# Performance work log

Measured on AMD Instinct MI355X. Metric: run time of the kernel, lower is better.

The kernel has to match this reference:

```python
import jax, jax.numpy as jnp
import numpy as np

IN_FEATURES = 4096
OUT_FEATURES = 4096
RANK = 16
ALPHA = 32.0
SCALING = ALPHA / RANK


def setup_inputs() -> dict:
    key = jax.random.key(0)
    k_x, k_a, k_b = jax.random.split(key, 3)
    x = jax.random.normal(k_x, (4, 2048, IN_FEATURES), dtype=jnp.float32)
    # kaiming-uniform(a=sqrt(5)) for A: bound = sqrt(6/((1+5)*fan_in)) = 1/sqrt(fan_in)
    bound = 1.0 / np.sqrt(IN_FEATURES)
    lora_A = jax.random.uniform(k_a, (RANK, IN_FEATURES), dtype=jnp.float32,
                                minval=-bound, maxval=bound)
    # B is zero-init in the module; use small random values so gradients are non-trivial
    lora_B = jax.random.normal(k_b, (OUT_FEATURES, RANK), dtype=jnp.float32) * 0.01
    return {"x": x, "lora_A": lora_A, "lora_B": lora_B}


def reference(x, lora_A, lora_B):
    # dropout=0 -> identity. F.linear(x, B@A) == x @ A^T @ B^T; keep low-rank order.
    h = jnp.einsum('bsd,rd->bsr', x, lora_A)      # [B,S,rank]
    out = jnp.einsum('bsr,or->bso', h, lora_B)    # [B,S,out_features]
    return out * SCALING
```

## Files before the change

kernel.cpp:

```cpp
#include <hip/hip_runtime.h>


#define IN_F  4096
#define OUT_F 4096
#define RANK  16
#define KSPLIT 32
#define KSLICE 128

__global__ __launch_bounds__(256) void k_transpose(const float* __restrict__ A,
                                                   float* __restrict__ At) {
    int idx = blockIdx.x * 256 + threadIdx.x;
    int r = idx >> 12;
    int k = idx & 4095;
    At[k * RANK + r] = A[idx];
}

__global__ __launch_bounds__(256) void k_stage1(const float* __restrict__ x,
                                                const float* __restrict__ At,
                                                float* __restrict__ hp) {
    const int tid  = threadIdx.x;
    const int w    = __builtin_amdgcn_readfirstlane(tid >> 6);
    const int lane = tid & 63;
    const int g    = blockIdx.x * 4 + w;
    const int rg   = g >> 5;
    const int ks   = g & (KSPLIT - 1);
    const size_t row = (size_t)rg * 64 + lane;
    const int k0   = ks * KSLICE;

    const float* xr = x + row * IN_F + k0;

    float p[RANK];
#pragma unroll
    for (int r = 0; r < RANK; ++r) p[r] = 0.0f;

#pragma unroll 2
    for (int c = 0; c < 8; ++c) {
        float4 v[4];
#pragma unroll
        for (int q = 0; q < 4; ++q)
            v[q] = *(const float4*)(xr + c * 16 + q * 4);
        const float* a = At + (size_t)(k0 + c * 16) * RANK;
#pragma unroll
        for (int q = 0; q < 4; ++q) {
            const float* aq = a + q * 64;
#pragma unroll
            for (int r = 0; r < RANK; ++r) p[r] += v[q].x * aq[r];
#pragma unroll
            for (int r = 0; r < RANK; ++r) p[r] += v[q].y * aq[RANK + r];
#pragma unroll
            for (int r = 0; r < RANK; ++r) p[r] += v[q].z * aq[2 * RANK + r];
#pragma unroll
            for (int r = 0; r < RANK; ++r) p[r] += v[q].w * aq[3 * RANK + r];
        }
    }

    float4* o = (float4*)(hp + ((size_t)ks * 8192 + row) * RANK);
    o[0] = make_float4(p[0],  p[1],  p[2],  p[3]);
    o[1] = make_float4(p[4],  p[5],  p[6],  p[7]);
    o[2] = make_float4(p[8],  p[9],  p[10], p[11]);
    o[3] = make_float4(p[12], p[13], p[14], p[15]);
}

__global__ __launch_bounds__(256) void k_stage2(const float* __restrict__ hp,
                                                const float* __restrict__ B,
                                                float* __restrict__ out) {
    __shared__ float hs[32 * RANK];
    const int tid  = threadIdx.x;
    const int b    = blockIdx.x;
    const int row0 = (b >> 2) * 32;
    const int col  = (b & 3) * 1024 + tid * 4;

#pragma unroll
    for (int i = 0; i < 2; ++i) {
        const int idx = i * 256 + tid;
        const float* src = hp + (size_t)row0 * RANK + idx;
        float s = 0.0f;
#pragma unroll
        for (int ks = 0; ks < KSPLIT; ++ks)
            s += src[(size_t)ks * 8192 * RANK];
        hs[idx] = 2.0f * s;
    }

    float4 breg[16];
    const float4* B4 = (const float4*)(B + (size_t)col * RANK);
#pragma unroll
    for (int i = 0; i < 16; ++i) breg[i] = B4[i];
    const float* bf = (const float*)breg;
    __syncthreads();

    for (int r = 0; r < 32; ++r) {
        const float4 h0 = *(const float4*)(hs + r * RANK);
        const float4 h1 = *(const float4*)(hs + r * RANK + 4);
        const float4 h2 = *(const float4*)(hs + r * RANK + 8);
        const float4 h3 = *(const float4*)(hs + r * RANK + 12);
        const float hv[16] = {h0.x, h0.y, h0.z, h0.w, h1.x, h1.y, h1.z, h1.w,
                              h2.x, h2.y, h2.z, h2.w, h3.x, h3.y, h3.z, h3.w};
        float4 acc = {0.f, 0.f, 0.f, 0.f};
#pragma unroll
        for (int rho = 0; rho < RANK; ++rho) {
            acc.x += hv[rho] * bf[0 * RANK + rho];
            acc.y += hv[rho] * bf[1 * RANK + rho];
            acc.z += hv[rho] * bf[2 * RANK + rho];
            acc.w += hv[rho] * bf[3 * RANK + rho];
        }
        *(float4*)(out + (size_t)(row0 + r) * OUT_F + col) = acc;
    }
}

extern "C" void kernel_launch(void* const* d_in, const int* in_sizes, int n_in,
                              void* d_out, int out_size, void* d_ws, size_t ws_size,
                              hipStream_t stream) {
    const float* x  = (const float*)d_in[0];
    const float* A  = (const float*)d_in[1];
    const float* Bm = (const float*)d_in[2];
    float* out = (float*)d_out;
    float* At  = (float*)d_ws;
    float* hp  = (float*)((char*)d_ws + (size_t)IN_F * RANK * 4);

    k_transpose<<<256, 256, 0, stream>>>(A, At);
    k_stage1<<<1024, 256, 0, stream>>>(x, At, hp);
    k_stage2<<<1024, 256, 0, stream>>>(hp, Bm, out);
}
```

Baseline: 291.2 us.

## Use split-bf16 MFMA for the down-projection and drop the transpose kernel

Stage 1 now computes x·A^T with bf16 MFMA instructions, splitting each fp32 value into high and low bf16 parts and issuing three MFMAs to keep close to fp32 accuracy. It reads A directly in MFMA fragment layout, which removes the separate transpose kernel. Stage 2 handles 16 rows per block and launches twice as many blocks. The aim is to move the scalar FMA work in stage 1 onto the matrix cores, at the cost of conversion arithmetic and some loss of accuracy. The up-projection (stage 2), which writes the large output, is unchanged apart from its block size.

Result: faster. 256.6 us (-11.9%).

```diff
diff --git a/kernel.cpp b/kernel.cpp
--- a/kernel.cpp
+++ b/kernel.cpp
@@ -7,16 +7,21 @@
 #define KSPLIT 32
 #define KSLICE 128
 
-__global__ __launch_bounds__(256) void k_transpose(const float* __restrict__ A,
-                                                   float* __restrict__ At) {
-    int idx = blockIdx.x * 256 + threadIdx.x;
-    int r = idx >> 12;
-    int k = idx & 4095;
-    At[k * RANK + r] = A[idx];
+typedef __attribute__((ext_vector_type(8))) short short8;
+typedef __attribute__((ext_vector_type(4))) float f32x4;
+
+static __device__ __forceinline__ short f2bf(float f) {
+    union { float f; unsigned u; } v; v.f = f;
+    unsigned r = v.u + 0x7fff + ((v.u >> 16) & 1);
+    return (short)(r >> 16);
+}
+static __device__ __forceinline__ float bf2f(short h) {
+    union { unsigned u; float f; } v; v.u = ((unsigned)(unsigned short)h) << 16;
+    return v.f;
 }
 
 __global__ __launch_bounds__(256) void k_stage1(const float* __restrict__ x,
-                                                const float* __restrict__ At,
+                                                const float* __restrict__ A,
                                                 float* __restrict__ hp) {
     const int tid  = threadIdx.x;
     const int w    = __builtin_amdgcn_readfirstlane(tid >> 6);
@@ -24,61 +29,82 @@
     const int g    = blockIdx.x * 4 + w;
     const int rg   = g >> 5;
     const int ks   = g & (KSPLIT - 1);
-    const size_t row = (size_t)rg * 64 + lane;
+    const int row0 = rg * 64;
     const int k0   = ks * KSLICE;
+    const int n    = lane & 15;
+    const int q    = lane >> 4;
 
-    const float* xr = x + row * IN_F + k0;
-
-    float p[RANK];
+    short8 Ahi[4], Alo[4];
 #pragma unroll
-    for (int r = 0; r < RANK; ++r) p[r] = 0.0f;
-
-#pragma unroll 2
-    for (int c = 0; c < 8; ++c) {
-        float4 v[4];
+    for (int kt = 0; kt < 4; ++kt) {
+        const float* ap = A + (size_t)n * IN_F + k0 + kt * 32 + q * 8;
+        const float4 a0 = *(const float4*)ap;
+        const float4 a1 = *(const float4*)(ap + 4);
+        const float av[8] = {a0.x, a0.y, a0.z, a0.w, a1.x, a1.y, a1.z, a1.w};
 #pragma unroll
-        for (int q = 0; q < 4; ++q)
-            v[q] = *(const float4*)(xr + c * 16 + q * 4);
-        const float* a = At + (size_t)(k0 + c * 16) * RANK;
-#pragma unroll
-        for (int q = 0; q < 4; ++q) {
-            const float* aq = a + q * 64;
-#pragma unroll
-            for (int r = 0; r < RANK; ++r) p[r] += v[q].x * aq[r];
-#pragma unroll
-            for (int r = 0; r < RANK; ++r) p[r] += v[q].y * aq[RANK + r];
-#pragma unroll
-            for (int r = 0; r < RANK; ++r) p[r] += v[q].z * aq[2 * RANK + r];
-#pragma unroll
-            for (int r = 0; r < RANK; ++r) p[r] += v[q].w * aq[3 * RANK + r];
+        for (int j = 0; j < 8; ++j) {
+            const short hi = f2bf(av[j]);
+            Ahi[kt][j] = hi;
+            Alo[kt][j] = f2bf(av[j] - bf2f(hi));
         }
     }
 
-    float4* o = (float4*)(hp + ((size_t)ks * 8192 + row) * RANK);
-    o[0] = make_float4(p[0],  p[1],  p[2],  p[3]);
-    o[1] = make_float4(p[4],  p[5],  p[6],  p[7]);
-    o[2] = make_float4(p[8],  p[9],  p[10], p[11]);
-    o[3] = make_float4(p[12], p[13], p[14], p[15]);
+    f32x4 acc[4];
+#pragma unroll
+    for (int rt = 0; rt < 4; ++rt) acc[rt] = (f32x4){0.f, 0.f, 0.f, 0.f};
+
+#pragma unroll
+    for (int rt = 0; rt < 4; ++rt) {
+        const float* xr = x + (size_t)(row0 + rt * 16 + n) * IN_F + k0 + q * 8;
+        float4 v0[4], v1[4];
+#pragma unroll
+        for (int kt = 0; kt < 4; ++kt) {
+            v0[kt] = *(const float4*)(xr + kt * 32);
+            v1[kt] = *(const float4*)(xr + kt * 32 + 4);
+        }
+#pragma unroll
+        for (int kt = 0; kt < 4; ++kt) {
+            const float xv[8] = {v0[kt].x, v0[kt].y, v0[kt].z, v0[kt].w,
+                                 v1[kt].x, v1[kt].y, v1[kt].z, v1[kt].w};
+            short8 xhi, xlo;
+#pragma unroll
+            for (int j = 0; j < 8; ++j) {
+                const short hi = f2bf(xv[j]);
+                xhi[j] = hi;
+                xlo[j] = f2bf(xv[j] - bf2f(hi));
+            }
+            acc[rt] = __builtin_amdgcn_mfma_f32_16x16x32_bf16(xhi, Ahi[kt], acc[rt], 0, 0, 0);
+            acc[rt] = __builtin_amdgcn_mfma_f32_16x16x32_bf16(xlo, Ahi[kt], acc[rt], 0, 0, 0);
+            acc[rt] = __builtin_amdgcn_mfma_f32_16x16x32_bf16(xhi, Alo[kt], acc[rt], 0, 0, 0);
+        }
+    }
+
+#pragma unroll
+    for (int rt = 0; rt < 4; ++rt) {
+#pragma unroll
+        for (int r = 0; r < 4; ++r) {
+            const int row = row0 + rt * 16 + q * 4 + r;
+            hp[((size_t)ks * 8192 + row) * RANK + n] = acc[rt][r];
+        }
+    }
 }
 
 __global__ __launch_bounds__(256) void k_stage2(const float* __restrict__ hp,
                                                 const float* __restrict__ B,
                                                 float* __restrict__ out) {
-    __shared__ float hs[32 * RANK];
+    __shared__ float hs[16 * RANK];
     const int tid  = threadIdx.x;
     const int b    = blockIdx.x;
-    const int row0 = (b >> 2) * 32;
+    const int row0 = (b >> 2) * 16;
     const int col  = (b & 3) * 1024 + tid * 4;
 
-#pragma unroll
-    for (int i = 0; i < 2; ++i) {
-        const int idx = i * 256 + tid;
-        const float* src = hp + (size_t)row0 * RANK + idx;
+    {
+        const float* src = hp + (size_t)row0 * RANK + tid;
         float s = 0.0f;
 #pragma unroll
         for (int ks = 0; ks < KSPLIT; ++ks)
             s += src[(size_t)ks * 8192 * RANK];
-        hs[idx] = 2.0f * s;
+        hs[tid] = 2.0f * s;
     }
 
     float4 breg[16];
@@ -88,7 +114,7 @@
     const float* bf = (const float*)breg;
     __syncthreads();
 
-    for (int r = 0; r < 32; ++r) {
+    for (int r = 0; r < 16; ++r) {
         const float4 h0 = *(const float4*)(hs + r * RANK);
         const float4 h1 = *(const float4*)(hs + r * RANK + 4);
         const float4 h2 = *(const float4*)(hs + r * RANK + 8);
@@ -114,10 +140,8 @@
     const float* A  = (const float*)d_in[1];
     const float* Bm = (const float*)d_in[2];
     float* out = (float*)d_out;
-    float* At  = (float*)d_ws;
-    float* hp  = (float*)((char*)d_ws + (size_t)IN_F * RANK * 4);
+    float* hp  = (float*)d_ws;
 
-    k_transpose<<<256, 256, 0, stream>>>(A, At);
-    k_stage1<<<1024, 256, 0, stream>>>(x, At, hp);
-    k_stage2<<<1024, 256, 0, stream>>>(hp, Bm, out);
+    k_stage1<<<1024, 256, 0, stream>>>(x, A, hp);
+    k_stage2<<<2048, 256, 0, stream>>>(hp, Bm, out);
 }
```
